# Kernel tuning notes

Measured on AMD Instinct MI355X. Metric: run time of the kernel, lower is better.

The kernel has to match this reference:

```python
import jax, jax.numpy as jnp
import numpy as np

B, N, C = 2, 2048, 768
H = 12
HD = C // H  # 64
EPS = 1e-6


def setup_inputs() -> dict:
    key = jax.random.key(0)
    ks = jax.random.split(key, 6)
    x = jax.random.normal(ks[0], (B, N, C), dtype=jnp.float32)
    # Xavier-uniform-ish init for kernels
    lim_qkv = float(np.sqrt(6.0 / (C + 3 * C)))
    lim_proj = float(np.sqrt(6.0 / (C + C)))
    qkv_kernel = jax.random.uniform(ks[1], (C, 3 * C), minval=-lim_qkv, maxval=lim_qkv, dtype=jnp.float32)
    qkv_bias = jnp.zeros((3 * C,), dtype=jnp.float32)
    proj_kernel = jax.random.uniform(ks[2], (C, C), minval=-lim_proj, maxval=lim_proj, dtype=jnp.float32)
    proj_bias = jnp.zeros((C,), dtype=jnp.float32)
    q_norm_w = jnp.ones((HD,), dtype=jnp.float32)
    k_norm_w = jnp.ones((HD,), dtype=jnp.float32)
    # Standard RoPE tables: freqs over half the head dim, tiled to full head_dim
    half = HD // 2
    inv_freq = 1.0 / (10000.0 ** (jnp.arange(0, half, dtype=jnp.float32) / half))
    t = jnp.arange(N, dtype=jnp.float32)
    freqs = jnp.outer(t, inv_freq)               # (N, HD/2)
    emb = jnp.concatenate([freqs, freqs], axis=-1)  # (N, HD)
    rope_cos = jnp.cos(emb)
    rope_sin = jnp.sin(emb)
    return {"x": x, "rope_cos": rope_cos, "rope_sin": rope_sin,
            "qkv_kernel": qkv_kernel, "qkv_bias": qkv_bias,
            "proj_kernel": proj_kernel, "proj_bias": proj_bias,
            "q_norm_w": q_norm_w, "k_norm_w": k_norm_w}


def _rms_norm(x, w):
    var = jnp.mean(x * x, axis=-1, keepdims=True)
    return x * jax.lax.rsqrt(var + EPS) * w


def _rope(x, cos, sin):
    # x: (B, H, N, HD); cos/sin: (N, HD)
    half = x.shape[-1] // 2
    x1, x2 = x[..., :half], x[..., half:]
    rot = jnp.concatenate([-x2, x1], axis=-1)
    return x * cos + rot * sin


def reference(x, rope_cos, rope_sin, qkv_kernel, qkv_bias, proj_kernel, proj_bias, q_norm_w, k_norm_w):
    b, n, c = x.shape
    qkv = x @ qkv_kernel + qkv_bias                       # (B, N, 3C)
    qkv = qkv.reshape(b, n, 3, H, HD).transpose(2, 0, 3, 1, 4)  # (3, B, H, N, HD)
    q, k, v = qkv[0], qkv[1], qkv[2]
    q = _rope(_rms_norm(q, q_norm_w), rope_cos, rope_sin)
    k = _rope(_rms_norm(k, k_norm_w), rope_cos, rope_sin)
    scale = 1.0 / jnp.sqrt(jnp.float32(HD)).astype(x.dtype)
    attn = jnp.einsum('bhqd,bhkd->bhqk', q, k) * scale    # (B, H, N, N)
    attn = jax.nn.softmax(attn, axis=-1)
    out = jnp.einsum('bhqk,bhkd->bhqd', attn, v)          # (B, H, N, HD)
    out = out.swapaxes(1, 2).reshape(b, n, c)
    return out @ proj_kernel + proj_bias
```

## Files before the change

kernel.cpp:

```cpp
#include <hip/hip_runtime.h>
#include <math.h>

#define B_    2
#define N_    2048
#define C_    768
#define H_    12
#define HD_   64
#define NROWS (B_*N_)
#define QKVC  (3*C_)
#define EPSV  1e-6f
#define SCALE 0.125f
#define LOG2E 1.44269504088896f
#define SMAX  12.0f

typedef unsigned short u16;
typedef short bf16x8 __attribute__((ext_vector_type(8)));
typedef float f32x4  __attribute__((ext_vector_type(4)));

__device__ __forceinline__ float b2f(u16 u) {
    unsigned v = ((unsigned)u) << 16;
    return __builtin_bit_cast(float, v);
}
__device__ __forceinline__ u16 f2b(float f) {
    unsigned u = __builtin_bit_cast(unsigned, f);
    u += 0x7fffu + ((u >> 16) & 1u);
    return (u16)(u >> 16);
}
__device__ __forceinline__ unsigned pk2(float a, float b) {
#if __has_builtin(__builtin_amdgcn_cvt_pk_bf16_f32)
    auto r = __builtin_amdgcn_cvt_pk_bf16_f32(a, b);
    return __builtin_bit_cast(unsigned, r);
#else
    return (unsigned)f2b(a) | ((unsigned)f2b(b) << 16);
#endif
}
__device__ __forceinline__ float fexp2(float x) {
#if __has_builtin(__builtin_amdgcn_exp2f)
    return __builtin_amdgcn_exp2f(x);
#else
    return exp2f(x);
#endif
}
__device__ __forceinline__ void gload_lds16(const void* g, void* l) {
    __builtin_amdgcn_global_load_lds(
        (const __attribute__((address_space(1))) unsigned int*)g,
        (__attribute__((address_space(3))) unsigned int*)l, 16, 0, 0);
}

__global__ __launch_bounds__(256)
void prep_kernel(const float* __restrict__ x,
                 const float* __restrict__ qkv_w,
                 const float* __restrict__ proj_w,
                 u16* __restrict__ xb,
                 u16* __restrict__ qwt,
                 u16* __restrict__ pwt) {
    __shared__ float T[64][65];
    const int t = threadIdx.x;
    if (blockIdx.x < 3072) {
        const int i = (blockIdx.x * 256 + t) * 4;
        const float4 v = *(const float4*)(x + i);
        uint2 o = { pk2(v.x, v.y), pk2(v.z, v.w) };
        *(uint2*)(xb + i) = o;
        return;
    }
    const float* W; u16* Wt; int K, N, k0, n0;
    if (blockIdx.x < 3072 + 432) {
        const int bx = blockIdx.x - 3072;
        W = qkv_w; Wt = qwt; K = C_; N = QKVC;
        n0 = (bx % 36) * 64; k0 = (bx / 36) * 64;
    } else {
        const int bx = blockIdx.x - 3504;
        W = proj_w; Wt = pwt; K = C_; N = C_;
        n0 = (bx % 12) * 64; k0 = (bx / 12) * 64;
    }
    const int r = t >> 6, c = t & 63;
#pragma unroll
    for (int p = 0; p < 16; ++p) {
        const int kl = p * 4 + r;
        T[kl][c] = W[(size_t)(k0 + kl) * N + n0 + c];
    }
    __syncthreads();
#pragma unroll
    for (int p = 0; p < 16; ++p) {
        const int nl = p * 4 + r;
        Wt[(size_t)(n0 + nl) * K + k0 + c] = f2b(T[c][nl]);
    }
}

template <bool BF16OUT>
__global__ __launch_bounds__(256)
void gemm_tn_kernel(const u16* __restrict__ A, const u16* __restrict__ Bt,
                    const float* __restrict__ bias, void* __restrict__ Cout,
                    int M, int N, int K) {
    __shared__ __attribute__((aligned(16))) u16 As[128 * 32];
    __shared__ __attribute__((aligned(16))) u16 Bs[128 * 32];
    const int tid = threadIdx.x;
    const int w = tid >> 6, l = tid & 63;
    const int lq = l & 15, quad = l >> 4;
    const int mbase = blockIdx.y * 128, nbase = blockIdx.x * 128;

    f32x4 acc[4][4];
    const f32x4 z4 = {0.f, 0.f, 0.f, 0.f};
#pragma unroll
    for (int mb = 0; mb < 4; ++mb)
#pragma unroll
        for (int nb = 0; nb < 4; ++nb) acc[mb][nb] = z4;

    const int srow = (l >> 2);
    const int sdc  = (l & 3) ^ ((l >> 2) & 3);

    for (int k0 = 0; k0 < K; k0 += 32) {
#pragma unroll
        for (int cc = 0; cc < 2; ++cc) {
            const int c = 2 * w + cc;
            const int row = 16 * c + srow;
            gload_lds16(A  + (size_t)(mbase + row) * K + k0 + sdc * 8, &As[c * 512]);
            gload_lds16(Bt + (size_t)(nbase + row) * K + k0 + sdc * 8, &Bs[c * 512]);
        }
        __syncthreads();

        bf16x8 af[4], bfr[4];
#pragma unroll
        for (int mb = 0; mb < 4; ++mb)
            af[mb] = *(const bf16x8*)
                &As[((w >> 1) * 64 + mb * 16 + lq) * 32 + ((quad ^ (lq & 3)) * 8)];
#pragma unroll
        for (int nb = 0; nb < 4; ++nb)
            bfr[nb] = *(const bf16x8*)
                &Bs[((w & 1) * 64 + nb * 16 + lq) * 32 + ((quad ^ (lq & 3)) * 8)];
#pragma unroll
        for (int mb = 0; mb < 4; ++mb)
#pragma unroll
            for (int nb = 0; nb < 4; ++nb)
                acc[mb][nb] = __builtin_amdgcn_mfma_f32_16x16x32_bf16(
                    af[mb], bfr[nb], acc[mb][nb], 0, 0, 0);
        __syncthreads();
    }

#pragma unroll
    for (int nb = 0; nb < 4; ++nb) {
        const int col = nbase + (w & 1) * 64 + nb * 16 + lq;
        const float bv = bias[col];
#pragma unroll
        for (int mb = 0; mb < 4; ++mb) {
#pragma unroll
            for (int r = 0; r < 4; ++r) {
                const int row = mbase + (w >> 1) * 64 + mb * 16 + quad * 4 + r;
                const float v = acc[mb][nb][r] + bv;
                if (BF16OUT) ((u16*)Cout)[(size_t)row * N + col] = f2b(v);
                else         ((float*)Cout)[(size_t)row * N + col] = v;
            }
        }
    }
}

__global__ __launch_bounds__(256)
void normrope_vpack_kernel(u16* __restrict__ qkv, u16* __restrict__ kpack,
                           u16* __restrict__ vpack,
                           const float* __restrict__ cosb,
                           const float* __restrict__ sinb,
                           const float* __restrict__ qw,
                           const float* __restrict__ kw) {
    if (blockIdx.x < 3072) {
        const int item = blockIdx.x * 16 + (threadIdx.x >> 4);
        const int lq   = threadIdx.x & 15;
        const int h    = item % H_;
        const int row  = item / H_;
        const int n    = row & (N_ - 1);
        const int b    = row >> 11;
        const size_t base = (size_t)row * QKVC + h * HD_ + lq * 4;

        const ushort4 q4 = *(const ushort4*)&qkv[base];
        const ushort4 k4 = *(const ushort4*)&qkv[base + C_];
        float qf[4], kf[4];
        qf[0] = b2f(q4.x); qf[1] = b2f(q4.y); qf[2] = b2f(q4.z); qf[3] = b2f(q4.w);
        kf[0] = b2f(k4.x); kf[1] = b2f(k4.y); kf[2] = b2f(k4.z); kf[3] = b2f(k4.w);

        float q2 = qf[0]*qf[0] + qf[1]*qf[1] + qf[2]*qf[2] + qf[3]*qf[3];
        float k2 = kf[0]*kf[0] + kf[1]*kf[1] + kf[2]*kf[2] + kf[3]*kf[3];
#pragma unroll
        for (int off = 8; off >= 1; off >>= 1) {
            q2 += __shfl_xor(q2, off, 64);
            k2 += __shfl_xor(k2, off, 64);
        }
        const float rq = rsqrtf(q2 * (1.f / 64.f) + EPSV);
        const float rk = rsqrtf(k2 * (1.f / 64.f) + EPSV);

        const float4 qwv = *(const float4*)&qw[lq * 4];
        const float4 kwv = *(const float4*)&kw[lq * 4];
        const float4 cv  = *(const float4*)&cosb[n * HD_ + lq * 4];
        const float4 sv  = *(const float4*)&sinb[n * HD_ + lq * 4];

        float qn[4], kn[4];
        qn[0] = qf[0]*rq*qwv.x; qn[1] = qf[1]*rq*qwv.y;
        qn[2] = qf[2]*rq*qwv.z; qn[3] = qf[3]*rq*qwv.w;
        kn[0] = kf[0]*rk*kwv.x; kn[1] = kf[1]*rk*kwv.y;
        kn[2] = kf[2]*rk*kwv.z; kn[3] = kf[3]*rk*kwv.w;

        const float sgn = (lq < 8) ? -1.f : 1.f;
        float qo[4], ko[4];
        const float cc[4] = {cv.x, cv.y, cv.z, cv.w};
        const float ss[4] = {sv.x, sv.y, sv.z, sv.w};
#pragma unroll
        for (int j = 0; j < 4; ++j) {
            const float qp = __shfl_xor(qn[j], 8, 64);
            const float kp = __shfl_xor(kn[j], 8, 64);
            qo[j] = (qn[j] * cc[j] + sgn * qp * ss[j]) * (SCALE * LOG2E);
            ko[j] =  kn[j] * cc[j] + sgn * kp * ss[j];
        }
        uint2 qout = { pk2(qo[0], qo[1]), pk2(qo[2], qo[3]) };
        uint2 kout = { pk2(ko[0], ko[1]), pk2(ko[2], ko[3]) };
        *(uint2*)&qkv[base] = qout;

        const int kt = n >> 6, kr = n & 63;
        const int kb = kr >> 4, m = kr & 15;
        const int ks = lq >> 3, quad = (lq >> 1) & 3, jj = (lq & 1) * 4;
        const size_t off = ((size_t)(b * H_ + h) * 32 + kt) * 4096
                         + (size_t)((kb * 2 + ks) * 64 + quad * 16 + m) * 8 + jj;
        *(uint2*)&kpack[off] = kout;
    } else {
        __shared__ u16 Tv[64][72];
        const int idx = blockIdx.x - 3072;
        const int kt = idx & 31, bh = idx >> 5;
        const int b = bh / H_, h = bh % H_;
        const int t = threadIdx.x;
        {
            const int r = t >> 2, seg = t & 3;
            const u16* src = &qkv[(size_t)(b * N_ + kt * 64 + r) * QKVC
                                  + 2 * C_ + h * HD_ + seg * 16];
            const uint4 v0 = *(const uint4*)src;
            const uint4 v1 = *(const uint4*)(src + 8);
            *(uint4*)&Tv[r][seg * 16]     = v0;
            *(uint4*)&Tv[r][seg * 16 + 8] = v1;
        }
        __syncthreads();
        u16 tmp[16];
#pragma unroll
        for (int g2 = 0; g2 < 2; ++g2) {
            const int g = t * 2 + g2;
            const int mbks = g >> 6;
            const int l  = g & 63;
            const int mb = mbks >> 1, ks = mbks & 1;
            const int m  = l & 15,  quad = l >> 4;
#pragma unroll
            for (int j = 0; j < 8; ++j)
                tmp[g2 * 8 + j] = Tv[ks * 32 + quad * 8 + j][mb * 16 + m];
        }
        u16* dst = &vpack[((size_t)bh * 32 + kt) * 4096 + t * 16];
        *(uint4*)dst       = *(const uint4*)&tmp[0];
        *(uint4*)(dst + 8) = *(const uint4*)&tmp[8];
    }
}

__global__ __launch_bounds__(128, 2)
void flash_mfma_kernel(const u16* __restrict__ qkv,
                       const u16* __restrict__ kpack,
                       const u16* __restrict__ vpack,
                       u16* __restrict__ opart,
                       float* __restrict__ lpart) {
    __shared__ __attribute__((aligned(16))) u16 Ps[2][64 * 64];
    __shared__ float lex[64];
    float* Oex = (float*)&Ps[0][0];

    const int tid = threadIdx.x;
    const int w = tid >> 6, l = tid & 63;
    const int lq = l & 15, quad = l >> 4;
    const int sw = lq & 7;

    const int lin  = blockIdx.x;
    const int slot = lin >> 3;
    const int bh   = (lin & 7) * 3 + (slot >> 6);
    const int rem  = slot & 63;
    const int qt   = rem >> 1;
    const int kh   = rem & 1;
    const int b = bh / H_, h = bh % H_;
    const size_t qbase = (size_t)b * N_ * QKVC + h * HD_;
    const size_t tbase = (size_t)bh * 32 * 4096;

    bf16x8 qb[4][2];
#pragma unroll
    for (int nq = 0; nq < 4; ++nq)
#pragma unroll
        for (int ks = 0; ks < 2; ++ks)
            qb[nq][ks] = *(const bf16x8*)
                &qkv[qbase + (size_t)(qt * 64 + nq * 16 + lq) * QKVC
                     + ks * 32 + quad * 8];

    float lsum[4] = {0.f, 0.f, 0.f, 0.f};
    f32x4 oacc[4][4];
    const f32x4 z4 = {0.f, 0.f, 0.f, 0.f};
#pragma unroll
    for (int mb = 0; mb < 4; ++mb)
#pragma unroll
        for (int nq = 0; nq < 4; ++nq) oacc[mb][nq] = z4;

    bf16x8 ka[4][2];
#pragma unroll
    for (int kb = 0; kb < 4; ++kb)
#pragma unroll
        for (int ks = 0; ks < 2; ++ks)
            ka[kb][ks] = *(const bf16x8*)
                &kpack[tbase + (size_t)(kh * 16 + w) * 4096
                       + ((kb * 2 + ks) * 64 + l) * 8];

    for (int kt2 = 0; kt2 < 8; ++kt2) {
        const int kt  = kh * 16 + 2 * kt2 + w;
        const int ktn = kh * 16 + ((2 * kt2 + 2 + w) & 15);
        const size_t vb   = tbase + (size_t)kt * 4096;
        const size_t kb_n = tbase + (size_t)ktn * 4096;

        bf16x8 va[4][2];
#pragma unroll
        for (int mb = 0; mb < 4; ++mb)
#pragma unroll
            for (int ks = 0; ks < 2; ++ks)
                va[mb][ks] = *(const bf16x8*)
                    &vpack[vb + ((mb * 2 + ks) * 64 + l) * 8];

#pragma unroll
        for (int kb = 0; kb < 4; ++kb) {
            f32x4 sacc[4];
#pragma unroll
            for (int nq = 0; nq < 4; ++nq) sacc[nq] = z4;
#pragma unroll
            for (int ks = 0; ks < 2; ++ks)
#pragma unroll
                for (int nq = 0; nq < 4; ++nq)
                    sacc[nq] = __builtin_amdgcn_mfma_f32_16x16x32_bf16(
                        ka[kb][ks], qb[nq][ks], sacc[nq], 0, 0, 0);
#pragma unroll
            for (int nq = 0; nq < 4; ++nq) {
                float p[4];
#pragma unroll
                for (int r = 0; r < 4; ++r) p[r] = fexp2(sacc[nq][r] - SMAX);
                lsum[nq] += (p[0] + p[1]) + (p[2] + p[3]);
                uint2 pkv = { pk2(p[0], p[1]), pk2(p[2], p[3]) };
                *(uint2*)&Ps[w][(nq * 16 + lq) * 64
                                + (((kb * 2 + (quad >> 1)) ^ sw) * 8)
                                + (quad & 1) * 4] = pkv;
            }
        }

#pragma unroll
        for (int kb = 0; kb < 4; ++kb)
#pragma unroll
            for (int ks = 0; ks < 2; ++ks)
                ka[kb][ks] = *(const bf16x8*)
                    &kpack[kb_n + ((kb * 2 + ks) * 64 + l) * 8];

        bf16x8 pb[2][4];
#pragma unroll
        for (int ks = 0; ks < 2; ++ks)
#pragma unroll
            for (int nq = 0; nq < 4; ++nq)
                pb[ks][nq] = *(const bf16x8*)
                    &Ps[w][(nq * 16 + lq) * 64 + (((ks * 4 + quad) ^ sw) * 8)];

#pragma unroll
        for (int mb = 0; mb < 4; ++mb)
#pragma unroll
            for (int ks = 0; ks < 2; ++ks)
#pragma unroll
                for (int nq = 0; nq < 4; ++nq)
                    oacc[mb][nq] = __builtin_amdgcn_mfma_f32_16x16x32_bf16(
                        va[mb][ks], pb[ks][nq], oacc[mb][nq], 0, 0, 0);
    }

#pragma unroll
    for (int nq = 0; nq < 4; ++nq) {
        lsum[nq] += __shfl_xor(lsum[nq], 16, 64);
        lsum[nq] += __shfl_xor(lsum[nq], 32, 64);
    }

    __syncthreads();
    if (w == 1) {
#pragma unroll
        for (int nq = 0; nq < 4; ++nq) {
#pragma unroll
            for (int mb = 0; mb < 4; ++mb) {
                const int chunkS = (mb * 4 + quad) ^ lq;
                float4 v;
                v.x = oacc[mb][nq][0]; v.y = oacc[mb][nq][1];
                v.z = oacc[mb][nq][2]; v.w = oacc[mb][nq][3];
                *(float4*)&Oex[(nq * 16 + lq) * 64 + chunkS * 4] = v;
            }
            if (quad == 0) lex[nq * 16 + lq] = lsum[nq];
        }
    }
    __syncthreads();
    if (w == 0) {
#pragma unroll
        for (int nq = 0; nq < 4; ++nq) {
#pragma unroll
            for (int mb = 0; mb < 4; ++mb) {
                const int chunkS = (mb * 4 + quad) ^ lq;
                float4* p = (float4*)&Oex[(nq * 16 + lq) * 64 + chunkS * 4];
                float4 v = *p;
                v.x += oacc[mb][nq][0]; v.y += oacc[mb][nq][1];
                v.z += oacc[mb][nq][2]; v.w += oacc[mb][nq][3];
                *p = v;
            }
            if (quad == 0) lex[nq * 16 + lq] += lsum[nq];
        }
    }
    __syncthreads();

    const size_t pbase_o = ((size_t)(bh * 32 + qt) * 2 + kh) * 4096;
    const size_t pbase_l = ((size_t)(bh * 32 + qt) * 2 + kh) * 64;
#pragma unroll
    for (int pass = 0; pass < 8; ++pass) {
        const int row = pass * 8 + (tid >> 4);
        const int c   = tid & 15;
        const int phys = c ^ (row & 15);
        const float4 v = *(const float4*)&Oex[row * 64 + phys * 4];
        uint2 o2 = { pk2(v.x, v.y), pk2(v.z, v.w) };
        *(uint2*)&opart[pbase_o + row * 64 + c * 4] = o2;
    }
    if (tid < 64) lpart[pbase_l + tid] = lex[tid];
}

__global__ __launch_bounds__(256)
void combine_kernel(const u16* __restrict__ opart,
                    const float* __restrict__ lpart,
                    u16* __restrict__ attnb) {
    const int lin  = blockIdx.x;
    const int slot = lin >> 3;
    const int bh   = (lin & 7) * 3 + (slot >> 5);
    const int qt   = slot & 31;
    const int b = bh / H_, h = bh % H_;
    const int t = threadIdx.x;
    const int q = t >> 2, g = t & 3;

    const size_t pair = (size_t)(bh * 32 + qt) * 2;
    const float lv = lpart[pair * 64 + q] + lpart[(pair + 1) * 64 + q];
    const float inv = 1.f / lv;

    const size_t p0 = pair * 4096 + q * 64 + g * 16;
    const size_t p1 = p0 + 4096;

    u16 res[16];
#pragma unroll
    for (int j4 = 0; j4 < 4; ++j4) {
        const ushort4 a = *(const ushort4*)&opart[p0 + j4 * 4];
        const ushort4 c = *(const ushort4*)&opart[p1 + j4 * 4];
        const float v0 = (b2f(a.x) + b2f(c.x)) * inv;
        const float v1 = (b2f(a.y) + b2f(c.y)) * inv;
        const float v2 = (b2f(a.z) + b2f(c.z)) * inv;
        const float v3 = (b2f(a.w) + b2f(c.w)) * inv;
        uint2 o2 = { pk2(v0, v1), pk2(v2, v3) };
        *(uint2*)&res[j4 * 4] = o2;
    }
    u16* dst = &attnb[(size_t)(b * N_ + qt * 64 + q) * C_ + h * HD_ + g * 16];
    *(uint4*)dst       = *(const uint4*)&res[0];
    *(uint4*)(dst + 8) = *(const uint4*)&res[8];
}

extern "C" void kernel_launch(void* const* d_in, const int* in_sizes, int n_in,
                              void* d_out, int out_size, void* d_ws, size_t ws_size,
                              hipStream_t stream) {
    const float* x        = (const float*)d_in[0];
    const float* rope_cos = (const float*)d_in[1];
    const float* rope_sin = (const float*)d_in[2];
    const float* qkv_w    = (const float*)d_in[3];
    const float* qkv_b    = (const float*)d_in[4];
    const float* proj_w   = (const float*)d_in[5];
    const float* proj_b   = (const float*)d_in[6];
    const float* q_nw     = (const float*)d_in[7];
    const float* k_nw     = (const float*)d_in[8];
    float* out = (float*)d_out;

    u16* xb     = (u16*)d_ws;
    u16* qwt    = xb     + (size_t)NROWS * C_;
    u16* pwt    = qwt    + (size_t)QKVC * C_;
    u16* qkvb   = pwt    + (size_t)C_ * C_;
    u16* vpackb = qkvb   + (size_t)NROWS * QKVC;
    u16* attnb  = vpackb + (size_t)B_ * H_ * 32 * 4096;
    u16* opartb = attnb  + (size_t)NROWS * C_;
    float* lpartb = (float*)(opartb + (size_t)1536 * 4096);
    u16* kpackb = xb;

    prep_kernel<<<dim3(3072 + 432 + 144), 256, 0, stream>>>(
        x, qkv_w, proj_w, xb, qwt, pwt);

    gemm_tn_kernel<true><<<dim3(QKVC / 128, NROWS / 128), 256, 0, stream>>>(
        xb, qwt, qkv_b, qkvb, NROWS, QKVC, C_);

    normrope_vpack_kernel<<<dim3(3072 + 768), 256, 0, stream>>>(
        qkvb, kpackb, vpackb, rope_cos, rope_sin, q_nw, k_nw);

    flash_mfma_kernel<<<dim3(1536), 128, 0, stream>>>(
        qkvb, kpackb, vpackb, opartb, lpartb);

    combine_kernel<<<dim3(768), 256, 0, stream>>>(opartb, lpartb, attnb);

    gemm_tn_kernel<false><<<dim3(C_ / 128, NROWS / 128), 256, 0, stream>>>(
        attnb, pwt, proj_b, out, NROWS, C_, C_);
}
```

Measured before the change: 207.4 us.

## Split norm-rope and KV packing, MFMA row sums, smaller proj GEMM tiles

Splits the fused norm/RoPE+V-pack kernel in two. Norm/RoPE now writes K back in place, and a new kernel packs both K and V through shared-memory transposes, adding a launch and an extra pass over K. In flash attention, the softmax denominator is now computed by an MFMA against a ones vector instead of scalar adds and shuffles, at the cost of extra matrix work. The output projection uses a new 64x64-tile, single-wave GEMM, giving 768 blocks instead of 192 so more CUs are busy.

New measurement: 208.9 us. About the same (+0.7%).

```diff
diff --git a/kernel.cpp b/kernel.cpp
--- a/kernel.cpp
+++ b/kernel.cpp
@@ -154,102 +154,165 @@
     }
 }
 
+__global__ __launch_bounds__(64)
+void gemm_tn64_kernel(const u16* __restrict__ A, const u16* __restrict__ Bt,
+                      const float* __restrict__ bias, float* __restrict__ Cout,
+                      int M, int N, int K) {
+    __shared__ __attribute__((aligned(16))) u16 As[64 * 32];
+    __shared__ __attribute__((aligned(16))) u16 Bs[64 * 32];
+    const int l = threadIdx.x;
+    const int lq = l & 15, quad = l >> 4;
+    const int mbase = blockIdx.y * 64, nbase = blockIdx.x * 64;
+
+    f32x4 acc[4][4];
+    const f32x4 z4 = {0.f, 0.f, 0.f, 0.f};
+#pragma unroll
+    for (int mb = 0; mb < 4; ++mb)
+#pragma unroll
+        for (int nb = 0; nb < 4; ++nb) acc[mb][nb] = z4;
+
+    const int srow = (l >> 2);
+    const int sdc  = (l & 3) ^ ((l >> 2) & 3);
+
+    for (int k0 = 0; k0 < K; k0 += 32) {
+#pragma unroll
+        for (int c = 0; c < 4; ++c) {
+            const int row = 16 * c + srow;
+            gload_lds16(A  + (size_t)(mbase + row) * K + k0 + sdc * 8, &As[c * 512]);
+            gload_lds16(Bt + (size_t)(nbase + row) * K + k0 + sdc * 8, &Bs[c * 512]);
+        }
+        __syncthreads();
+
+        bf16x8 af[4], bfr[4];
+#pragma unroll
+        for (int mb = 0; mb < 4; ++mb)
+            af[mb] = *(const bf16x8*)
+                &As[(mb * 16 + lq) * 32 + ((quad ^ (lq & 3)) * 8)];
+#pragma unroll
+        for (int nb = 0; nb < 4; ++nb)
+            bfr[nb] = *(const bf16x8*)
+                &Bs[(nb * 16 + lq) * 32 + ((quad ^ (lq & 3)) * 8)];
+#pragma unroll
+        for (int mb = 0; mb < 4; ++mb)
+#pragma unroll
+            for (int nb = 0; nb < 4; ++nb)
+                acc[mb][nb] = __builtin_amdgcn_mfma_f32_16x16x32_bf16(
+                    af[mb], bfr[nb], acc[mb][nb], 0, 0, 0);
+        __syncthreads();
+    }
+
+#pragma unroll
+    for (int nb = 0; nb < 4; ++nb) {
+        const int col = nbase + nb * 16 + lq;
+        const float bv = bias[col];
+#pragma unroll
+        for (int mb = 0; mb < 4; ++mb) {
+#pragma unroll
+            for (int r = 0; r < 4; ++r) {
+                const int row = mbase + mb * 16 + quad * 4 + r;
+                Cout[(size_t)row * N + col] = acc[mb][nb][r] + bv;
+            }
+        }
+    }
+}
+
 __global__ __launch_bounds__(256)
-void normrope_vpack_kernel(u16* __restrict__ qkv, u16* __restrict__ kpack,
-                           u16* __restrict__ vpack,
-                           const float* __restrict__ cosb,
-                           const float* __restrict__ sinb,
-                           const float* __restrict__ qw,
-                           const float* __restrict__ kw) {
-    if (blockIdx.x < 3072) {
-        const int item = blockIdx.x * 16 + (threadIdx.x >> 4);
-        const int lq   = threadIdx.x & 15;
-        const int h    = item % H_;
-        const int row  = item / H_;
-        const int n    = row & (N_ - 1);
-        const int b    = row >> 11;
-        const size_t base = (size_t)row * QKVC + h * HD_ + lq * 4;
-
-        const ushort4 q4 = *(const ushort4*)&qkv[base];
-        const ushort4 k4 = *(const ushort4*)&qkv[base + C_];
-        float qf[4], kf[4];
-        qf[0] = b2f(q4.x); qf[1] = b2f(q4.y); qf[2] = b2f(q4.z); qf[3] = b2f(q4.w);
-        kf[0] = b2f(k4.x); kf[1] = b2f(k4.y); kf[2] = b2f(k4.z); kf[3] = b2f(k4.w);
-
-        float q2 = qf[0]*qf[0] + qf[1]*qf[1] + qf[2]*qf[2] + qf[3]*qf[3];
-        float k2 = kf[0]*kf[0] + kf[1]*kf[1] + kf[2]*kf[2] + kf[3]*kf[3];
-#pragma unroll
-        for (int off = 8; off >= 1; off >>= 1) {
-            q2 += __shfl_xor(q2, off, 64);
-            k2 += __shfl_xor(k2, off, 64);
-        }
-        const float rq = rsqrtf(q2 * (1.f / 64.f) + EPSV);
-        const float rk = rsqrtf(k2 * (1.f / 64.f) + EPSV);
-
-        const float4 qwv = *(const float4*)&qw[lq * 4];
-        const float4 kwv = *(const float4*)&kw[lq * 4];
-        const float4 cv  = *(const float4*)&cosb[n * HD_ + lq * 4];
-        const float4 sv  = *(const float4*)&sinb[n * HD_ + lq * 4];
-
-        float qn[4], kn[4];
-        qn[0] = qf[0]*rq*qwv.x; qn[1] = qf[1]*rq*qwv.y;
-        qn[2] = qf[2]*rq*qwv.z; qn[3] = qf[3]*rq*qwv.w;
-        kn[0] = kf[0]*rk*kwv.x; kn[1] = kf[1]*rk*kwv.y;
-        kn[2] = kf[2]*rk*kwv.z; kn[3] = kf[3]*rk*kwv.w;
-
-        const float sgn = (lq < 8) ? -1.f : 1.f;
-        float qo[4], ko[4];
-        const float cc[4] = {cv.x, cv.y, cv.z, cv.w};
-        const float ss[4] = {sv.x, sv.y, sv.z, sv.w};
-#pragma unroll
-        for (int j = 0; j < 4; ++j) {
-            const float qp = __shfl_xor(qn[j], 8, 64);
-            const float kp = __shfl_xor(kn[j], 8, 64);
-            qo[j] = (qn[j] * cc[j] + sgn * qp * ss[j]) * (SCALE * LOG2E);
-            ko[j] =  kn[j] * cc[j] + sgn * kp * ss[j];
-        }
-        uint2 qout = { pk2(qo[0], qo[1]), pk2(qo[2], qo[3]) };
-        uint2 kout = { pk2(ko[0], ko[1]), pk2(ko[2], ko[3]) };
-        *(uint2*)&qkv[base] = qout;
-
-        const int kt = n >> 6, kr = n & 63;
-        const int kb = kr >> 4, m = kr & 15;
-        const int ks = lq >> 3, quad = (lq >> 1) & 3, jj = (lq & 1) * 4;
-        const size_t off = ((size_t)(b * H_ + h) * 32 + kt) * 4096
-                         + (size_t)((kb * 2 + ks) * 64 + quad * 16 + m) * 8 + jj;
-        *(uint2*)&kpack[off] = kout;
-    } else {
-        __shared__ u16 Tv[64][72];
-        const int idx = blockIdx.x - 3072;
-        const int kt = idx & 31, bh = idx >> 5;
-        const int b = bh / H_, h = bh % H_;
-        const int t = threadIdx.x;
-        {
-            const int r = t >> 2, seg = t & 3;
-            const u16* src = &qkv[(size_t)(b * N_ + kt * 64 + r) * QKVC
-                                  + 2 * C_ + h * HD_ + seg * 16];
-            const uint4 v0 = *(const uint4*)src;
-            const uint4 v1 = *(const uint4*)(src + 8);
-            *(uint4*)&Tv[r][seg * 16]     = v0;
-            *(uint4*)&Tv[r][seg * 16 + 8] = v1;
-        }
-        __syncthreads();
-        u16 tmp[16];
-#pragma unroll
-        for (int g2 = 0; g2 < 2; ++g2) {
-            const int g = t * 2 + g2;
-            const int mbks = g >> 6;
-            const int l  = g & 63;
-            const int mb = mbks >> 1, ks = mbks & 1;
-            const int m  = l & 15,  quad = l >> 4;
-#pragma unroll
-            for (int j = 0; j < 8; ++j)
-                tmp[g2 * 8 + j] = Tv[ks * 32 + quad * 8 + j][mb * 16 + m];
-        }
-        u16* dst = &vpack[((size_t)bh * 32 + kt) * 4096 + t * 16];
-        *(uint4*)dst       = *(const uint4*)&tmp[0];
-        *(uint4*)(dst + 8) = *(const uint4*)&tmp[8];
-    }
+void normrope_kernel(u16* __restrict__ qkv,
+                     const float* __restrict__ cosb,
+                     const float* __restrict__ sinb,
+                     const float* __restrict__ qw,
+                     const float* __restrict__ kw) {
+    const int item = blockIdx.x * 16 + (threadIdx.x >> 4);
+    const int lq   = threadIdx.x & 15;
+    const int h    = item % H_;
+    const int row  = item / H_;
+    const int n    = row & (N_ - 1);
+    const size_t base = (size_t)row * QKVC + h * HD_ + lq * 4;
+
+    const ushort4 q4 = *(const ushort4*)&qkv[base];
+    const ushort4 k4 = *(const ushort4*)&qkv[base + C_];
+    float qf[4], kf[4];
+    qf[0] = b2f(q4.x); qf[1] = b2f(q4.y); qf[2] = b2f(q4.z); qf[3] = b2f(q4.w);
+    kf[0] = b2f(k4.x); kf[1] = b2f(k4.y); kf[2] = b2f(k4.z); kf[3] = b2f(k4.w);
+
+    float q2 = qf[0]*qf[0] + qf[1]*qf[1] + qf[2]*qf[2] + qf[3]*qf[3];
+    float k2 = kf[0]*kf[0] + kf[1]*kf[1] + kf[2]*kf[2] + kf[3]*kf[3];
+#pragma unroll
+    for (int off = 8; off >= 1; off >>= 1) {
+        q2 += __shfl_xor(q2, off, 64);
+        k2 += __shfl_xor(k2, off, 64);
+    }
+    const float rq = rsqrtf(q2 * (1.f / 64.f) + EPSV);
+    const float rk = rsqrtf(k2 * (1.f / 64.f) + EPSV);
+
+    const float4 qwv = *(const float4*)&qw[lq * 4];
+    const float4 kwv = *(const float4*)&kw[lq * 4];
+    const float4 cv  = *(const float4*)&cosb[n * HD_ + lq * 4];
+    const float4 sv  = *(const float4*)&sinb[n * HD_ + lq * 4];
+
+    float qn[4], kn[4];
+    qn[0] = qf[0]*rq*qwv.x; qn[1] = qf[1]*rq*qwv.y;
+    qn[2] = qf[2]*rq*qwv.z; qn[3] = qf[3]*rq*qwv.w;
+    kn[0] = kf[0]*rk*kwv.x; kn[1] = kf[1]*rk*kwv.y;
+    kn[2] = kf[2]*rk*kwv.z; kn[3] = kf[3]*rk*kwv.w;
+
+    const float sgn = (lq < 8) ? -1.f : 1.f;
+    float qo[4], ko[4];
+    const float cc[4] = {cv.x, cv.y, cv.z, cv.w};
+    const float ss[4] = {sv.x, sv.y, sv.z, sv.w};
+#pragma unroll
+    for (int j = 0; j < 4; ++j) {
+        const float qp = __shfl_xor(qn[j], 8, 64);
+        const float kp = __shfl_xor(kn[j], 8, 64);
+        qo[j] = (qn[j] * cc[j] + sgn * qp * ss[j]) * (SCALE * LOG2E);
+        ko[j] =  kn[j] * cc[j] + sgn * kp * ss[j];
+    }
+    uint2 qout = { pk2(qo[0], qo[1]), pk2(qo[2], qo[3]) };
+    uint2 kout = { pk2(ko[0], ko[1]), pk2(ko[2], ko[3]) };
+    *(uint2*)&qkv[base]      = qout;
+    *(uint2*)&qkv[base + C_] = kout;
+}
+
+__global__ __launch_bounds__(256)
+void kvpack_kernel(const u16* __restrict__ qkv,
+                   u16* __restrict__ kpack, u16* __restrict__ vpack) {
+    __shared__ u16 Tk[64][72];
+    __shared__ u16 Tv[64][72];
+    const int kt = blockIdx.x & 31, bh = blockIdx.x >> 5;
+    const int b = bh / H_, h = bh % H_;
+    const int t = threadIdx.x;
+    {
+        const int r = t >> 2, seg = t & 3;
+        const u16* srck = &qkv[(size_t)(b * N_ + kt * 64 + r) * QKVC
+                               + C_ + h * HD_ + seg * 16];
+        *(uint4*)&Tk[r][seg * 16]     = *(const uint4*)srck;
+        *(uint4*)&Tk[r][seg * 16 + 8] = *(const uint4*)(srck + 8);
+        const u16* srcv = srck + C_;
+        *(uint4*)&Tv[r][seg * 16]     = *(const uint4*)srcv;
+        *(uint4*)&Tv[r][seg * 16 + 8] = *(const uint4*)(srcv + 8);
+    }
+    __syncthreads();
+    const size_t tile = ((size_t)bh * 32 + kt) * 4096;
+    u16 ktmp[16], vtmp[16];
+#pragma unroll
+    for (int g2 = 0; g2 < 2; ++g2) {
+        const int g = t * 2 + g2;
+        const int blk = g >> 6;
+        const int l  = g & 63;
+        const int bb = blk >> 1, ks = blk & 1;
+        const int m  = l & 15,  quad = l >> 4;
+#pragma unroll
+        for (int j = 0; j < 8; ++j) {
+            ktmp[g2 * 8 + j] = Tk[bb * 16 + m][ks * 32 + quad * 8 + j];
+            vtmp[g2 * 8 + j] = Tv[ks * 32 + quad * 8 + j][bb * 16 + m];
+        }
+    }
+    u16* kd = &kpack[tile + t * 16];
+    *(uint4*)kd       = *(const uint4*)&ktmp[0];
+    *(uint4*)(kd + 8) = *(const uint4*)&ktmp[8];
+    u16* vd = &vpack[tile + t * 16];
+    *(uint4*)vd       = *(const uint4*)&vtmp[0];
+    *(uint4*)(vd + 8) = *(const uint4*)&vtmp[8];
 }
 
 __global__ __launch_bounds__(128, 2)
@@ -277,6 +340,14 @@
     const size_t qbase = (size_t)b * N_ * QKVC + h * HD_;
     const size_t tbase = (size_t)bh * 32 * 4096;
 
+    bf16x8 onesf;
+    {
+        const short one = (short)0x3F80;
+        const short v = (lq == 0) ? one : (short)0;
+#pragma unroll
+        for (int j = 0; j < 8; ++j) onesf[j] = v;
+    }
+
     bf16x8 qb[4][2];
 #pragma unroll
     for (int nq = 0; nq < 4; ++nq)
@@ -286,13 +357,14 @@
                 &qkv[qbase + (size_t)(qt * 64 + nq * 16 + lq) * QKVC
                      + ks * 32 + quad * 8];
 
-    float lsum[4] = {0.f, 0.f, 0.f, 0.f};
-    f32x4 oacc[4][4];
+    f32x4 oacc[4][4], lacc[4];
     const f32x4 z4 = {0.f, 0.f, 0.f, 0.f};
 #pragma unroll
     for (int mb = 0; mb < 4; ++mb)
 #pragma unroll
         for (int nq = 0; nq < 4; ++nq) oacc[mb][nq] = z4;
+#pragma unroll
+    for (int nq = 0; nq < 4; ++nq) lacc[nq] = z4;
 
     bf16x8 ka[4][2];
 #pragma unroll
@@ -333,7 +405,6 @@
                 float p[4];
 #pragma unroll
                 for (int r = 0; r < 4; ++r) p[r] = fexp2(sacc[nq][r] - SMAX);
-                lsum[nq] += (p[0] + p[1]) + (p[2] + p[3]);
                 uint2 pkv = { pk2(p[0], p[1]), pk2(p[2], p[3]) };
                 *(uint2*)&Ps[w][(nq * 16 + lq) * 64
                                 + (((kb * 2 + (quad >> 1)) ^ sw) * 8)
@@ -364,13 +435,14 @@
                 for (int nq = 0; nq < 4; ++nq)
                     oacc[mb][nq] = __builtin_amdgcn_mfma_f32_16x16x32_bf16(
                         va[mb][ks], pb[ks][nq], oacc[mb][nq], 0, 0, 0);
-    }
-
-#pragma unroll
-    for (int nq = 0; nq < 4; ++nq) {
-        lsum[nq] += __shfl_xor(lsum[nq], 16, 64);
-        lsum[nq] += __shfl_xor(lsum[nq], 32, 64);
-    }
+#pragma unroll
+        for (int ks = 0; ks < 2; ++ks)
+#pragma unroll
+            for (int nq = 0; nq < 4; ++nq)
+                lacc[nq] = __builtin_amdgcn_mfma_f32_16x16x32_bf16(
+                    onesf, pb[ks][nq], lacc[nq], 0, 0, 0);
+    }
+
 
     __syncthreads();
     if (w == 1) {
@@ -384,7 +456,7 @@
                 v.z = oacc[mb][nq][2]; v.w = oacc[mb][nq][3];
                 *(float4*)&Oex[(nq * 16 + lq) * 64 + chunkS * 4] = v;
             }
-            if (quad == 0) lex[nq * 16 + lq] = lsum[nq];
+            if (quad == 0) lex[nq * 16 + lq] = lacc[nq][0];
         }
     }
     __syncthreads();
@@ -400,7 +472,7 @@
                 v.z += oacc[mb][nq][2]; v.w += oacc[mb][nq][3];
                 *p = v;
             }
-            if (quad == 0) lex[nq * 16 + lq] += lsum[nq];
+            if (quad == 0) lex[nq * 16 + lq] += lacc[nq][0];
         }
     }
     __syncthreads();
@@ -485,14 +557,16 @@
     gemm_tn_kernel<true><<<dim3(QKVC / 128, NROWS / 128), 256, 0, stream>>>(
         xb, qwt, qkv_b, qkvb, NROWS, QKVC, C_);
 
-    normrope_vpack_kernel<<<dim3(3072 + 768), 256, 0, stream>>>(
-        qkvb, kpackb, vpackb, rope_cos, rope_sin, q_nw, k_nw);
+    normrope_kernel<<<dim3(3072), 256, 0, stream>>>(
+        qkvb, rope_cos, rope_sin, q_nw, k_nw);
+
+    kvpack_kernel<<<dim3(768), 256, 0, stream>>>(qkvb, kpackb, vpackb);
 
     flash_mfma_kernel<<<dim3(1536), 128, 0, stream>>>(
         qkvb, kpackb, vpackb, opartb, lpartb);
 
     combine_kernel<<<dim3(768), 256, 0, stream>>>(opartb, lpartb, attnb);
 
-    gemm_tn_kernel<false><<<dim3(C_ / 128, NROWS / 128), 256, 0, stream>>>(
+    gemm_tn64_kernel<<<dim3(C_ / 64, NROWS / 64), 64, 0, stream>>>(
         attnb, pwt, proj_b, out, NROWS, C_, C_);
 }
```
